# Kernel optimization log

Hardware: AMD Instinct MI355X
Metric: run time of the kernel (lower is better)

Reference implementation:

```python
import jax, jax.numpy as jnp
import numpy as np

N_USERS = 100000
N_ENT = 100000
DIM = 64
HID = 128
E = 1600000
B = 8192


def _renorm(emb, max_norm=1.0):
    # torch nn.Embedding(max_norm=1): rows are rescaled to norm <= max_norm on lookup
    n = jnp.linalg.norm(emb, axis=-1, keepdims=True)
    return emb * jnp.minimum(1.0, max_norm / jnp.maximum(n, 1e-12))


def _gcn_conv(x, W, b, src, dst, n):
    # PyG GCNConv: h = x W; add self-loops; sym-normalized scatter-add; + bias
    h = x @ W  # [n, out]
    deg = jax.ops.segment_sum(jnp.ones(src.shape, jnp.float32), dst, num_segments=n) + 1.0  # self-loop
    dinv = jax.lax.rsqrt(deg)
    norm = (dinv[src] * dinv[dst])[:, None]  # [E,1]
    out = jax.ops.segment_sum(h[src] * norm, dst, num_segments=n)
    out = out + h * (1.0 / deg)[:, None]  # self-loop term: deg^-1/2 * deg^-1/2 = 1/deg
    return out + b


def setup_inputs() -> dict:
    key = jax.random.key(0)
    ks = jax.random.split(key, 8)
    return {
        "u": jax.random.randint(ks[0], (B,), 0, N_USERS),
        "i": jax.random.randint(ks[1], (B,), 0, N_ENT),
        "edges": jax.random.randint(ks[2], (2, E), 0, N_ENT),
        "user_emb": jax.random.normal(ks[3], (N_USERS, DIM), jnp.float32) * 0.1,
        "entity_emb": jax.random.normal(ks[4], (N_ENT, DIM), jnp.float32) * 0.1,
        "W1": jax.random.normal(ks[5], (DIM, HID), jnp.float32) * (1.0 / np.sqrt(DIM)),
        "b1": jnp.zeros((HID,), jnp.float32),
        "W2": jax.random.normal(ks[6], (HID, DIM), jnp.float32) * (1.0 / np.sqrt(HID)),
        "b2": jnp.zeros((DIM,), jnp.float32),
    }


def reference(u, i, edges, user_emb, entity_emb, W1, b1, W2, b2):
    src, dst = edges[0], edges[1]
    n = entity_emb.shape[0]
    x = _renorm(entity_emb)  # entitys(all_entitys_indexes) with max_norm=1
    x = jax.nn.relu(_gcn_conv(x, W1, b1, src, dst, n))  # dropout = identity (eval)
    x = _gcn_conv(x, W2, b2, src, dst, n)
    items = x[i]  # [B, DIM]
    users = _renorm(user_emb)[u]  # [B, DIM]
    uv = jnp.sum(users * items, axis=1)
    return jax.nn.sigmoid(uv)
```

## Files before the change

kernel.cpp:

```cpp
#include <hip/hip_runtime.h>
#include <hip/hip_bf16.h>
#include <math.h>

constexpr int N_ENT = 100000;
constexpr int NEDGE = 1600000;
constexpr int BATCH = 8192;

constexpr int NBUCK   = 256;
constexpr int KNODE   = 391;
constexpr int TILE    = 4096;
constexpr int NTILE   = (NEDGE + TILE - 1) / TILE;
constexpr int BUCKCAP = 8192;

constexpr int NBLK_G = (N_ENT + 63) / 64;
constexpr int ZROWS  = NBLK_G * 64;


typedef __attribute__((ext_vector_type(8))) short bf16x8;
typedef __attribute__((ext_vector_type(4))) float f32x4;

__device__ inline unsigned short f2b(float x) {
    unsigned int u = __float_as_uint(x);
    unsigned int r = (u + 0x7fffu + ((u >> 16) & 1u)) >> 16;
    return (unsigned short)r;
}
__device__ inline float blo(unsigned int p) { return __uint_as_float(p << 16); }
__device__ inline float bhi(unsigned int p) { return __uint_as_float(p & 0xffff0000u); }


__global__ __launch_bounds__(256) void ginit_k(int* __restrict__ gcursor) {
    gcursor[threadIdx.x] = threadIdx.x * BUCKCAP;
}

__global__ __launch_bounds__(256) void bin_k(const int* __restrict__ edges,
                                             int* __restrict__ gcursor,
                                             unsigned int* __restrict__ temp) {
    __shared__ int cnt[NBUCK];
    __shared__ int gb[NBUCK];
    __shared__ int off[NBUCK];
    int tid  = threadIdx.x;
    int base = blockIdx.x * TILE;
    unsigned int val[16];
    unsigned int bpk[4] = {0u, 0u, 0u, 0u};
    cnt[tid] = 0;
    __syncthreads();
#pragma unroll
    for (int i = 0; i < 16; ++i) {
        int e = base + i * 256 + tid;
        unsigned int b = 0u;
        if (e < NEDGE) {
            int s  = edges[e];
            int d  = edges[NEDGE + e];
            int bb = d / KNODE;
            int dl = d - bb * KNODE;
            val[i] = ((unsigned int)s << 9) | (unsigned int)dl;
            b = (unsigned int)bb;
            atomicAdd(&cnt[bb], 1);
        } else {
            val[i] = 0xffffffffu;
        }
        bpk[i >> 2] |= b << ((i & 3) * 8);
    }
    __syncthreads();
    if (cnt[tid] > 0) gb[tid] = atomicAdd(&gcursor[tid], cnt[tid]);
    off[tid] = 0;
    __syncthreads();
#pragma unroll
    for (int i = 0; i < 16; ++i) {
        if (val[i] != 0xffffffffu) {
            int b = (int)((bpk[i >> 2] >> ((i & 3) * 8)) & 255u);
            int p = atomicAdd(&off[b], 1);
            temp[gb[b] + p] = val[i];
        }
    }
}

__global__ __launch_bounds__(256) void unbinC_k(const unsigned int* __restrict__ temp,
                                                const int* __restrict__ gcursor,
                                                const float* __restrict__ W1g,
                                                const float* __restrict__ W2g,
                                                uint4* __restrict__ w1p,
                                                uint4* __restrict__ w2p,
                                                int* __restrict__ row_start,
                                                int* __restrict__ srcs) {
    __shared__ unsigned int st[BUCKCAP];
    __shared__ int bs[NBUCK];
    __shared__ int cnt[KNODE];
    __shared__ int cur[KNODE];
    int b   = blockIdx.x;
    int tid = threadIdx.x;
    if (b >= NBUCK) {
        int t    = (b - NBUCK) * 256 + tid;
        int e    = t & 1023;
        int lane = e & 63, cs = e >> 6;
        int li   = lane & 15, quad = lane >> 4;
        unsigned short v[8];
        if (t < 1024) {
            int ct = cs >> 1, s = cs & 1;
            int kb = s * 32 + quad * 8;
            int n  = ct * 16 + li;
#pragma unroll
            for (int j = 0; j < 8; ++j) v[j] = f2b(W1g[(kb + j) * 128 + n]);
            uint4 p;
            p.x = (unsigned)v[0] | ((unsigned)v[1] << 16);
            p.y = (unsigned)v[2] | ((unsigned)v[3] << 16);
            p.z = (unsigned)v[4] | ((unsigned)v[5] << 16);
            p.w = (unsigned)v[6] | ((unsigned)v[7] << 16);
            w1p[e] = p;
        } else {
            int ct = cs >> 2, s = cs & 3;
            int kb = s * 32 + quad * 8;
            int n  = ct * 16 + li;
#pragma unroll
            for (int j = 0; j < 8; ++j) v[j] = f2b(W2g[(kb + j) * 64 + n]);
            uint4 p;
            p.x = (unsigned)v[0] | ((unsigned)v[1] << 16);
            p.y = (unsigned)v[2] | ((unsigned)v[3] << 16);
            p.z = (unsigned)v[4] | ((unsigned)v[5] << 16);
            p.w = (unsigned)v[6] | ((unsigned)v[7] << 16);
            w2p[e] = p;
        }
        return;
    }
    int myc = gcursor[tid] - tid * BUCKCAP;
    bs[tid] = myc;
    __syncthreads();
    for (int off = 1; off < NBUCK; off <<= 1) {
        int x = (tid >= off) ? bs[tid - off] : 0;
        __syncthreads();
        bs[tid] += x;
        __syncthreads();
    }
    int node0 = b * KNODE;
    int nn    = N_ENT - node0; if (nn > KNODE) nn = KNODE;
    int tbeg  = b * BUCKCAP;
    int m     = gcursor[b] - tbeg;
    int bucket_base = bs[b] - m;
    for (int i = tid; i < KNODE; i += 256) cnt[i] = 0;
    __syncthreads();
    for (int i = tid; i < m; i += 256) {
        unsigned int x = temp[tbeg + i];
        st[i] = x;
        atomicAdd(&cnt[x & 511u], 1);
    }
    if (b == 0 && tid == 255) row_start[N_ENT] = NEDGE;
    __syncthreads();
    if (tid < 64) {
        int lane = tid;
        int loc[7];
        int s = 0;
#pragma unroll
        for (int j = 0; j < 7; ++j) {
            int idx = lane * 7 + j;
            int d = (idx < nn) ? cnt[idx] : 0;
            loc[j] = s;
            s += d;
        }
        int v = s;
#pragma unroll
        for (int o = 1; o < 64; o <<= 1) {
            int x = __shfl_up(v, o, 64);
            if (lane >= o) v += x;
        }
        int pfx = v - s;
#pragma unroll
        for (int j = 0; j < 7; ++j) {
            int idx = lane * 7 + j;
            if (idx < nn) {
                int rs = bucket_base + pfx + loc[j];
                cur[idx] = rs;
                row_start[node0 + idx] = rs;
            }
        }
    }
    __syncthreads();
    for (int i = tid; i < m; i += 256) {
        unsigned int x = st[i];
        int dl  = (int)(x & 511u);
        int pos = atomicAdd(&cur[dl], 1);
        srcs[pos] = (int)(x >> 9);
    }
}

__global__ __launch_bounds__(256) void prep_k(const float* __restrict__ emb,
                                              const int* __restrict__ row_start,
                                              float* __restrict__ dinv,
                                              unsigned short* __restrict__ emb_b) {
    int gt   = blockIdx.x * 256 + threadIdx.x;
    int n    = gt >> 6;
    int lane = threadIdx.x & 63;
    if (n > N_ENT) return;
    if (n == N_ENT) { emb_b[(size_t)n * 64 + lane] = 0; return; }
    float v = emb[(size_t)n * 64 + lane];
    float s = v * v;
#pragma unroll
    for (int o = 32; o > 0; o >>= 1) s += __shfl_xor(s, o, 64);
    float nrm = sqrtf(s);
    float sc  = nrm > 1.0f ? 1.0f / nrm : 1.0f;
    int   deg = row_start[n + 1] - row_start[n];
    float dv  = 1.0f / sqrtf((float)(deg + 1));
    if (lane == 0) dinv[n] = dv;
    emb_b[(size_t)n * 64 + lane] = f2b(sc * dv * v);
}

__global__ __launch_bounds__(256) void reduce1_k(int dst0,
                                                 const int* __restrict__ row_start,
                                                 const int* __restrict__ srcs,
                                                 const unsigned short* __restrict__ emb_b,
                                                 const float* __restrict__ dinv,
                                                 unsigned short* __restrict__ zb) {
    int gt   = blockIdx.x * 256 + threadIdx.x;
    int dst  = dst0 + (gt >> 6);
    int lane = threadIdx.x & 63;
    int sub  = lane >> 4;
    int li   = lane & 15;
    int beg = row_start[dst];
    int end = row_start[dst + 1];
    float4 acc = make_float4(0.f, 0.f, 0.f, 0.f);
    for (int base = beg; base < end; base += 64) {
        int cnt = end - base; if (cnt > 64) cnt = 64;
        int s_v = (base + lane < end) ? srcs[base + lane] : N_ENT;
        for (int jj = 0; jj < cnt; jj += 16) {
            int s0 = __shfl(s_v, jj + sub,      64);
            int s1 = __shfl(s_v, jj + 4 + sub,  64);
            int s2 = __shfl(s_v, jj + 8 + sub,  64);
            int s3 = __shfl(s_v, jj + 12 + sub, 64);
            uint2 p0 = *(const uint2*)(emb_b + (size_t)s0 * 64 + li * 4);
            uint2 p1 = *(const uint2*)(emb_b + (size_t)s1 * 64 + li * 4);
            uint2 p2 = *(const uint2*)(emb_b + (size_t)s2 * 64 + li * 4);
            uint2 p3 = *(const uint2*)(emb_b + (size_t)s3 * 64 + li * 4);
            acc.x += blo(p0.x) + blo(p1.x) + blo(p2.x) + blo(p3.x);
            acc.y += bhi(p0.x) + bhi(p1.x) + bhi(p2.x) + bhi(p3.x);
            acc.z += blo(p0.y) + blo(p1.y) + blo(p2.y) + blo(p3.y);
            acc.w += bhi(p0.y) + bhi(p1.y) + bhi(p2.y) + bhi(p3.y);
        }
    }
    acc.x += __shfl_xor(acc.x, 16, 64); acc.y += __shfl_xor(acc.y, 16, 64);
    acc.z += __shfl_xor(acc.z, 16, 64); acc.w += __shfl_xor(acc.w, 16, 64);
    acc.x += __shfl_xor(acc.x, 32, 64); acc.y += __shfl_xor(acc.y, 32, 64);
    acc.z += __shfl_xor(acc.z, 32, 64); acc.w += __shfl_xor(acc.w, 32, 64);
    if (lane < 16) {
        uint2 po = *(const uint2*)(emb_b + (size_t)dst * 64 + li * 4);
        float dv = dinv[dst];
        unsigned int h0 = f2b(dv * (acc.x + blo(po.x)));
        unsigned int h1 = f2b(dv * (acc.y + bhi(po.x)));
        unsigned int h2 = f2b(dv * (acc.z + blo(po.y)));
        unsigned int h3 = f2b(dv * (acc.w + bhi(po.y)));
        uint2 p;
        p.x = h0 | (h1 << 16);
        p.y = h2 | (h3 << 16);
        *(uint2*)(zb + (size_t)dst * 64 + li * 4) = p;
    }
}

__global__ __launch_bounds__(256) void mlp_k(const unsigned short* __restrict__ zb,
                                             const uint4* __restrict__ w1p,
                                             const float* __restrict__ b1,
                                             const uint4* __restrict__ w2p,
                                             const float* __restrict__ dinv,
                                             unsigned short* __restrict__ h2b) {
    __shared__ unsigned short y1s[4][16 * 136];
    __shared__ unsigned short h2s[4][16 * 64];
    int tid  = threadIdx.x;
    int w    = tid >> 6, lane = tid & 63;
    int li   = lane & 15, quad = lane >> 4;
    int r0   = blockIdx.x * 64 + w * 16;
    uint4 a0u = *(const uint4*)(zb + (size_t)(r0 + li) * 64 + quad * 8);
    uint4 a1u = *(const uint4*)(zb + (size_t)(r0 + li) * 64 + 32 + quad * 8);
    bf16x8 a0 = *(bf16x8*)&a0u;
    bf16x8 a1 = *(bf16x8*)&a1u;
    unsigned short* ys = y1s[w];
#pragma unroll
    for (int ct = 0; ct < 8; ++ct) {
        uint4 b0u = w1p[(ct * 2 + 0) * 64 + lane];
        uint4 b1u = w1p[(ct * 2 + 1) * 64 + lane];
        f32x4 acc = {0.f, 0.f, 0.f, 0.f};
        acc = __builtin_amdgcn_mfma_f32_16x16x32_bf16(a0, *(bf16x8*)&b0u, acc, 0, 0, 0);
        acc = __builtin_amdgcn_mfma_f32_16x16x32_bf16(a1, *(bf16x8*)&b1u, acc, 0, 0, 0);
        float bias = b1[ct * 16 + li];
#pragma unroll
        for (int r = 0; r < 4; ++r)
            ys[(quad * 4 + r) * 136 + ct * 16 + li] = f2b(fmaxf(acc[r] + bias, 0.f));
    }
    __syncthreads();
    bf16x8 a2[4];
#pragma unroll
    for (int s = 0; s < 4; ++s) {
        uint4 au = *(const uint4*)(ys + li * 136 + s * 32 + quad * 8);
        a2[s] = *(bf16x8*)&au;
    }
    float dvr[4];
#pragma unroll
    for (int r = 0; r < 4; ++r) {
        int grow = r0 + quad * 4 + r;
        dvr[r] = (grow < N_ENT) ? dinv[grow] : 0.f;
    }
    unsigned short* hs = h2s[w];
#pragma unroll
    for (int ct = 0; ct < 4; ++ct) {
        f32x4 acc = {0.f, 0.f, 0.f, 0.f};
#pragma unroll
        for (int s = 0; s < 4; ++s) {
            uint4 bu = w2p[(ct * 4 + s) * 64 + lane];
            acc = __builtin_amdgcn_mfma_f32_16x16x32_bf16(a2[s], *(bf16x8*)&bu, acc, 0, 0, 0);
        }
#pragma unroll
        for (int r = 0; r < 4; ++r)
            hs[(quad * 4 + r) * 64 + ct * 16 + li] = f2b(acc[r] * dvr[r]);
    }
    __syncthreads();
#pragma unroll
    for (int q = 0; q < 2; ++q) {
        int t4   = lane * 2 + q;
        int rl   = t4 >> 3;
        int c0   = (t4 & 7) * 8;
        int grow = r0 + rl;
        if (grow < N_ENT) {
            *(uint4*)(h2b + (size_t)grow * 64 + c0) = *(const uint4*)(hs + rl * 64 + c0);
        } else if (grow == N_ENT) {
            uint4 zz; zz.x = 0u; zz.y = 0u; zz.z = 0u; zz.w = 0u;
            *(uint4*)(h2b + (size_t)grow * 64 + c0) = zz;
        }
    }
}

__global__ __launch_bounds__(256) void reduce2f_k(const int* __restrict__ u,
                                                  const int* __restrict__ iidx,
                                                  const float* __restrict__ uemb,
                                                  const int* __restrict__ row_start,
                                                  const int* __restrict__ srcs,
                                                  const unsigned short* __restrict__ h2b,
                                                  const float* __restrict__ dinv,
                                                  const float* __restrict__ b2,
                                                  float* __restrict__ out) {
    int gt   = blockIdx.x * 256 + threadIdx.x;
    int b    = gt >> 6;
    int lane = threadIdx.x & 63;
    int sub  = lane >> 4;
    int li   = lane & 15;
    int dst = iidx[b];
    int beg = row_start[dst];
    int end = row_start[dst + 1];
    float4 acc = make_float4(0.f, 0.f, 0.f, 0.f);
    for (int base = beg; base < end; base += 64) {
        int cnt = end - base; if (cnt > 64) cnt = 64;
        int s_v = (base + lane < end) ? srcs[base + lane] : N_ENT;
        for (int jj = 0; jj < cnt; jj += 16) {
            int s0 = __shfl(s_v, jj + sub,      64);
            int s1 = __shfl(s_v, jj + 4 + sub,  64);
            int s2 = __shfl(s_v, jj + 8 + sub,  64);
            int s3 = __shfl(s_v, jj + 12 + sub, 64);
            uint2 p0 = *(const uint2*)(h2b + (size_t)s0 * 64 + li * 4);
            uint2 p1 = *(const uint2*)(h2b + (size_t)s1 * 64 + li * 4);
            uint2 p2 = *(const uint2*)(h2b + (size_t)s2 * 64 + li * 4);
            uint2 p3 = *(const uint2*)(h2b + (size_t)s3 * 64 + li * 4);
            acc.x += blo(p0.x) + blo(p1.x) + blo(p2.x) + blo(p3.x);
            acc.y += bhi(p0.x) + bhi(p1.x) + bhi(p2.x) + bhi(p3.x);
            acc.z += blo(p0.y) + blo(p1.y) + blo(p2.y) + blo(p3.y);
            acc.w += bhi(p0.y) + bhi(p1.y) + bhi(p2.y) + bhi(p3.y);
        }
    }
    acc.x += __shfl_xor(acc.x, 16, 64); acc.y += __shfl_xor(acc.y, 16, 64);
    acc.z += __shfl_xor(acc.z, 16, 64); acc.w += __shfl_xor(acc.w, 16, 64);
    acc.x += __shfl_xor(acc.x, 32, 64); acc.y += __shfl_xor(acc.y, 32, 64);
    acc.z += __shfl_xor(acc.z, 32, 64); acc.w += __shfl_xor(acc.w, 32, 64);
    float s1 = 0.f, s2 = 0.f;
    if (lane < 16) {
        uint2 po = *(const uint2*)(h2b + (size_t)dst * 64 + li * 4);
        float dv = dinv[dst];
        float4 bb = *(const float4*)(b2 + li * 4);
        float4 z2v;
        z2v.x = dv * (acc.x + blo(po.x)) + bb.x;
        z2v.y = dv * (acc.y + bhi(po.x)) + bb.y;
        z2v.z = dv * (acc.z + blo(po.y)) + bb.z;
        z2v.w = dv * (acc.w + bhi(po.y)) + bb.w;
        float4 ue = *(const float4*)(uemb + (size_t)u[b] * 64 + li * 4);
        s1 = ue.x * ue.x + ue.y * ue.y + ue.z * ue.z + ue.w * ue.w;
        s2 = ue.x * z2v.x + ue.y * z2v.y + ue.z * z2v.z + ue.w * z2v.w;
    }
#pragma unroll
    for (int o = 8; o > 0; o >>= 1) {
        s1 += __shfl_xor(s1, o, 64);
        s2 += __shfl_xor(s2, o, 64);
    }
    if (lane == 0) {
        float nrm = sqrtf(s1);
        float sc  = nrm > 1.0f ? 1.0f / nrm : 1.0f;
        float uv  = s2 * sc;
        out[b] = 1.0f / (1.0f + expf(-uv));
    }
}

extern "C" void kernel_launch(void* const* d_in, const int* in_sizes, int n_in,
                              void* d_out, int out_size, void* d_ws, size_t ws_size,
                              hipStream_t stream) {
    const int*   u          = (const int*)d_in[0];
    const int*   iidx       = (const int*)d_in[1];
    const int*   edges      = (const int*)d_in[2];
    const float* user_emb   = (const float*)d_in[3];
    const float* entity_emb = (const float*)d_in[4];
    const float* W1         = (const float*)d_in[5];
    const float* b1         = (const float*)d_in[6];
    const float* W2         = (const float*)d_in[7];
    const float* b2         = (const float*)d_in[8];
    float*       out        = (float*)d_out;

    char* ws = (char*)d_ws;
    float*          dinv      = (float*)         (ws + 100000u * 4);
    int*            row_start = (int*)           (ws + 200000u * 4);
    int*            gcursor   = (int*)           (ws + 300004u * 4);
    uint4*          w1p       = (uint4*)         (ws + 300656u * 4);
    uint4*          w2p       = (uint4*)         (ws + 304752u * 4);
    int*            srcs      = (int*)           (ws + 308848u * 4);
    unsigned short* emb_b     = (unsigned short*)(ws + 1908848u * 4);
    unsigned short* zb        = (unsigned short*)(ws + 3508864u * 4);
    unsigned short* h2b       = (unsigned short*)(ws + 6711936u * 4);
    unsigned int*   temp      = (unsigned int*)  (ws + 8311968u * 4);

    ginit_k<<<1, 256, 0, stream>>>(gcursor);
    bin_k<<<NTILE, 256, 0, stream>>>(edges, gcursor, temp);
    unbinC_k<<<NBUCK + 8, 256, 0, stream>>>(temp, gcursor, W1, W2, w1p, w2p,
                                            row_start, srcs);
    prep_k<<<N_ENT * 64 / 256 + 1, 256, 0, stream>>>(entity_emb, row_start,
                                                     dinv, emb_b);

    reduce1_k<<<12500, 256, 0, stream>>>(0,     row_start, srcs, emb_b, dinv, zb);
    reduce1_k<<<12500, 256, 0, stream>>>(50000, row_start, srcs, emb_b, dinv, zb);
    mlp_k<<<NBLK_G, 256, 0, stream>>>(zb, w1p, b1, w2p, dinv, h2b);

    reduce2f_k<<<BATCH * 64 / 256, 256, 0, stream>>>(u, iidx, user_emb, row_start,
                                                     srcs, h2b, dinv, b2, out);
}
```

Baseline: 234.2 us.

## Fuse graph preprocessing kernels into one cooperative kernel with grid syncs

Merges cursor init, edge binning, CSR build with weight packing, and embedding renorm/bf16 conversion into a single cooperative kernel separated by grid.sync barriers. It also merges the two reduce1 launches into one and vectorizes the prep stage to float4 loads. The aim is to cut kernel launch overhead and inter-kernel gaps. In exchange, the grid is limited to NTILE blocks that must all be co-resident, and the CSR phase runs on only a subset of them while the rest wait at the barrier.

After: 377.7 us. +61.3%, slower.

```diff
diff --git a/kernel.cpp b/kernel.cpp
--- a/kernel.cpp
+++ b/kernel.cpp
@@ -1,6 +1,9 @@
 #include <hip/hip_runtime.h>
 #include <hip/hip_bf16.h>
+#include <hip/hip_cooperative_groups.h>
 #include <math.h>
+
+namespace cg = cooperative_groups;
 
 constexpr int N_ENT = 100000;
 constexpr int NEDGE = 1600000;
@@ -13,7 +16,6 @@
 constexpr int BUCKCAP = 8192;
 
 constexpr int NBLK_G = (N_ENT + 63) / 64;
-constexpr int ZROWS  = NBLK_G * 64;
 
 
 typedef __attribute__((ext_vector_type(8))) short bf16x8;
@@ -28,68 +30,129 @@
 __device__ inline float bhi(unsigned int p) { return __uint_as_float(p & 0xffff0000u); }
 
 
-__global__ __launch_bounds__(256) void ginit_k(int* __restrict__ gcursor) {
-    gcursor[threadIdx.x] = threadIdx.x * BUCKCAP;
-}
-
-__global__ __launch_bounds__(256) void bin_k(const int* __restrict__ edges,
+__global__ __launch_bounds__(256) void pre_k(const int* __restrict__ edges,
+                                             const float* __restrict__ W1g,
+                                             const float* __restrict__ W2g,
+                                             uint4* __restrict__ w1p,
+                                             uint4* __restrict__ w2p,
                                              int* __restrict__ gcursor,
-                                             unsigned int* __restrict__ temp) {
-    __shared__ int cnt[NBUCK];
-    __shared__ int gb[NBUCK];
-    __shared__ int off[NBUCK];
-    int tid  = threadIdx.x;
-    int base = blockIdx.x * TILE;
-    unsigned int val[16];
-    unsigned int bpk[4] = {0u, 0u, 0u, 0u};
-    cnt[tid] = 0;
-    __syncthreads();
-#pragma unroll
-    for (int i = 0; i < 16; ++i) {
-        int e = base + i * 256 + tid;
-        unsigned int b = 0u;
-        if (e < NEDGE) {
-            int s  = edges[e];
-            int d  = edges[NEDGE + e];
-            int bb = d / KNODE;
-            int dl = d - bb * KNODE;
-            val[i] = ((unsigned int)s << 9) | (unsigned int)dl;
-            b = (unsigned int)bb;
-            atomicAdd(&cnt[bb], 1);
-        } else {
-            val[i] = 0xffffffffu;
-        }
-        bpk[i >> 2] |= b << ((i & 3) * 8);
-    }
-    __syncthreads();
-    if (cnt[tid] > 0) gb[tid] = atomicAdd(&gcursor[tid], cnt[tid]);
-    off[tid] = 0;
-    __syncthreads();
-#pragma unroll
-    for (int i = 0; i < 16; ++i) {
-        if (val[i] != 0xffffffffu) {
-            int b = (int)((bpk[i >> 2] >> ((i & 3) * 8)) & 255u);
-            int p = atomicAdd(&off[b], 1);
-            temp[gb[b] + p] = val[i];
-        }
-    }
-}
-
-__global__ __launch_bounds__(256) void unbinC_k(const unsigned int* __restrict__ temp,
-                                                const int* __restrict__ gcursor,
-                                                const float* __restrict__ W1g,
-                                                const float* __restrict__ W2g,
-                                                uint4* __restrict__ w1p,
-                                                uint4* __restrict__ w2p,
-                                                int* __restrict__ row_start,
-                                                int* __restrict__ srcs) {
+                                             unsigned int* __restrict__ temp,
+                                             int* __restrict__ row_start,
+                                             int* __restrict__ srcs,
+                                             const float* __restrict__ emb,
+                                             float* __restrict__ dinv,
+                                             unsigned short* __restrict__ emb_b) {
+    cg::grid_group grid = cg::this_grid();
     __shared__ unsigned int st[BUCKCAP];
-    __shared__ int bs[NBUCK];
-    __shared__ int cnt[KNODE];
-    __shared__ int cur[KNODE];
+    __shared__ int cntS[KNODE];
+    __shared__ int curS[KNODE];
+    __shared__ int bsS[NBUCK];
     int b   = blockIdx.x;
     int tid = threadIdx.x;
-    if (b >= NBUCK) {
+
+    if (b == 0) {
+        gcursor[tid] = tid * BUCKCAP;
+        if (tid == 0) row_start[N_ENT] = NEDGE;
+    }
+    grid.sync();
+
+    {
+        int base = b * TILE;
+        unsigned int val[16];
+        unsigned int bpk[4] = {0u, 0u, 0u, 0u};
+        cntS[tid] = 0;
+        __syncthreads();
+#pragma unroll
+        for (int i = 0; i < 16; ++i) {
+            int e = base + i * 256 + tid;
+            unsigned int bk = 0u;
+            if (e < NEDGE) {
+                int s  = edges[e];
+                int d  = edges[NEDGE + e];
+                int bb = d / KNODE;
+                int dl = d - bb * KNODE;
+                val[i] = ((unsigned int)s << 9) | (unsigned int)dl;
+                bk = (unsigned int)bb;
+                atomicAdd(&cntS[bb], 1);
+            } else {
+                val[i] = 0xffffffffu;
+            }
+            bpk[i >> 2] |= bk << ((i & 3) * 8);
+        }
+        __syncthreads();
+        if (cntS[tid] > 0) curS[tid] = atomicAdd(&gcursor[tid], cntS[tid]);
+        bsS[tid] = 0;
+        __syncthreads();
+#pragma unroll
+        for (int i = 0; i < 16; ++i) {
+            if (val[i] != 0xffffffffu) {
+                int bk = (int)((bpk[i >> 2] >> ((i & 3) * 8)) & 255u);
+                int p  = atomicAdd(&bsS[bk], 1);
+                temp[curS[bk] + p] = val[i];
+            }
+        }
+    }
+    grid.sync();
+
+    if (b < NBUCK) {
+        int myc = gcursor[tid] - tid * BUCKCAP;
+        bsS[tid] = myc;
+        __syncthreads();
+        for (int off = 1; off < NBUCK; off <<= 1) {
+            int x = (tid >= off) ? bsS[tid - off] : 0;
+            __syncthreads();
+            bsS[tid] += x;
+            __syncthreads();
+        }
+        int node0 = b * KNODE;
+        int nn    = N_ENT - node0; if (nn > KNODE) nn = KNODE;
+        int tbeg  = b * BUCKCAP;
+        int m     = gcursor[b] - tbeg;
+        int bucket_base = bsS[b] - m;
+        for (int i = tid; i < KNODE; i += 256) cntS[i] = 0;
+        __syncthreads();
+        for (int i = tid; i < m; i += 256) {
+            unsigned int x = temp[tbeg + i];
+            st[i] = x;
+            atomicAdd(&cntS[x & 511u], 1);
+        }
+        __syncthreads();
+        if (tid < 64) {
+            int lane = tid;
+            int loc[7];
+            int s = 0;
+#pragma unroll
+            for (int j = 0; j < 7; ++j) {
+                int idx = lane * 7 + j;
+                int d = (idx < nn) ? cntS[idx] : 0;
+                loc[j] = s;
+                s += d;
+            }
+            int v = s;
+#pragma unroll
+            for (int o = 1; o < 64; o <<= 1) {
+                int x = __shfl_up(v, o, 64);
+                if (lane >= o) v += x;
+            }
+            int pfx = v - s;
+#pragma unroll
+            for (int j = 0; j < 7; ++j) {
+                int idx = lane * 7 + j;
+                if (idx < nn) {
+                    int rs = bucket_base + pfx + loc[j];
+                    curS[idx] = rs;
+                    row_start[node0 + idx] = rs;
+                }
+            }
+        }
+        __syncthreads();
+        for (int i = tid; i < m; i += 256) {
+            unsigned int x = st[i];
+            int dl  = (int)(x & 511u);
+            int pos = atomicAdd(&curS[dl], 1);
+            srcs[pos] = (int)(x >> 9);
+        }
+    } else if (b < NBUCK + 8) {
         int t    = (b - NBUCK) * 256 + tid;
         int e    = t & 1023;
         int lane = e & 63, cs = e >> 6;
@@ -120,97 +183,54 @@
             p.w = (unsigned)v[6] | ((unsigned)v[7] << 16);
             w2p[e] = p;
         }
-        return;
-    }
-    int myc = gcursor[tid] - tid * BUCKCAP;
-    bs[tid] = myc;
-    __syncthreads();
-    for (int off = 1; off < NBUCK; off <<= 1) {
-        int x = (tid >= off) ? bs[tid - off] : 0;
-        __syncthreads();
-        bs[tid] += x;
-        __syncthreads();
-    }
-    int node0 = b * KNODE;
-    int nn    = N_ENT - node0; if (nn > KNODE) nn = KNODE;
-    int tbeg  = b * BUCKCAP;
-    int m     = gcursor[b] - tbeg;
-    int bucket_base = bs[b] - m;
-    for (int i = tid; i < KNODE; i += 256) cnt[i] = 0;
-    __syncthreads();
-    for (int i = tid; i < m; i += 256) {
-        unsigned int x = temp[tbeg + i];
-        st[i] = x;
-        atomicAdd(&cnt[x & 511u], 1);
-    }
-    if (b == 0 && tid == 255) row_start[N_ENT] = NEDGE;
-    __syncthreads();
-    if (tid < 64) {
-        int lane = tid;
-        int loc[7];
-        int s = 0;
-#pragma unroll
-        for (int j = 0; j < 7; ++j) {
-            int idx = lane * 7 + j;
-            int d = (idx < nn) ? cnt[idx] : 0;
-            loc[j] = s;
-            s += d;
-        }
-        int v = s;
-#pragma unroll
-        for (int o = 1; o < 64; o <<= 1) {
-            int x = __shfl_up(v, o, 64);
-            if (lane >= o) v += x;
-        }
-        int pfx = v - s;
-#pragma unroll
-        for (int j = 0; j < 7; ++j) {
-            int idx = lane * 7 + j;
-            if (idx < nn) {
-                int rs = bucket_base + pfx + loc[j];
-                cur[idx] = rs;
-                row_start[node0 + idx] = rs;
-            }
-        }
-    }
-    __syncthreads();
-    for (int i = tid; i < m; i += 256) {
-        unsigned int x = st[i];
-        int dl  = (int)(x & 511u);
-        int pos = atomicAdd(&cur[dl], 1);
-        srcs[pos] = (int)(x >> 9);
-    }
-}
-
-__global__ __launch_bounds__(256) void prep_k(const float* __restrict__ emb,
-                                              const int* __restrict__ row_start,
-                                              float* __restrict__ dinv,
-                                              unsigned short* __restrict__ emb_b) {
-    int gt   = blockIdx.x * 256 + threadIdx.x;
-    int n    = gt >> 6;
-    int lane = threadIdx.x & 63;
-    if (n > N_ENT) return;
-    if (n == N_ENT) { emb_b[(size_t)n * 64 + lane] = 0; return; }
-    float v = emb[(size_t)n * 64 + lane];
-    float s = v * v;
-#pragma unroll
-    for (int o = 32; o > 0; o >>= 1) s += __shfl_xor(s, o, 64);
-    float nrm = sqrtf(s);
-    float sc  = nrm > 1.0f ? 1.0f / nrm : 1.0f;
-    int   deg = row_start[n + 1] - row_start[n];
-    float dv  = 1.0f / sqrtf((float)(deg + 1));
-    if (lane == 0) dinv[n] = dv;
-    emb_b[(size_t)n * 64 + lane] = f2b(sc * dv * v);
-}
-
-__global__ __launch_bounds__(256) void reduce1_k(int dst0,
-                                                 const int* __restrict__ row_start,
+    }
+    grid.sync();
+
+    {
+        int lane  = tid & 63;
+        int qid   = lane >> 4, li = lane & 15;
+        int gw    = (b * 256 + tid) >> 6;
+        int nw    = (NTILE * 256) >> 6;
+        for (int n4 = gw; n4 <= N_ENT / 4; n4 += nw) {
+            int n = n4 * 4 + qid;
+            if (n > N_ENT) continue;
+            unsigned short* dst = emb_b + (size_t)n * 64 + li * 4;
+            if (n == N_ENT) {
+                uint2 z; z.x = 0u; z.y = 0u;
+                *(uint2*)dst = z;
+                continue;
+            }
+            float4 v = *(const float4*)(emb + (size_t)n * 64 + li * 4);
+            float s = v.x * v.x + v.y * v.y + v.z * v.z + v.w * v.w;
+            s += __shfl_xor(s, 1, 64);
+            s += __shfl_xor(s, 2, 64);
+            s += __shfl_xor(s, 4, 64);
+            s += __shfl_xor(s, 8, 64);
+            float nrm = sqrtf(s);
+            float sc  = nrm > 1.0f ? 1.0f / nrm : 1.0f;
+            int   deg = row_start[n + 1] - row_start[n];
+            float dv  = 1.0f / sqrtf((float)(deg + 1));
+            if (li == 0) dinv[n] = dv;
+            float mch = sc * dv;
+            unsigned int h0 = f2b(mch * v.x);
+            unsigned int h1 = f2b(mch * v.y);
+            unsigned int h2 = f2b(mch * v.z);
+            unsigned int h3 = f2b(mch * v.w);
+            uint2 p;
+            p.x = h0 | (h1 << 16);
+            p.y = h2 | (h3 << 16);
+            *(uint2*)dst = p;
+        }
+    }
+}
+
+__global__ __launch_bounds__(256) void reduce1_k(const int* __restrict__ row_start,
                                                  const int* __restrict__ srcs,
                                                  const unsigned short* __restrict__ emb_b,
                                                  const float* __restrict__ dinv,
                                                  unsigned short* __restrict__ zb) {
     int gt   = blockIdx.x * 256 + threadIdx.x;
-    int dst  = dst0 + (gt >> 6);
+    int dst  = gt >> 6;
     int lane = threadIdx.x & 63;
     int sub  = lane >> 4;
     int li   = lane & 15;
@@ -417,15 +437,25 @@
     unsigned short* h2b       = (unsigned short*)(ws + 6711936u * 4);
     unsigned int*   temp      = (unsigned int*)  (ws + 8311968u * 4);
 
-    ginit_k<<<1, 256, 0, stream>>>(gcursor);
-    bin_k<<<NTILE, 256, 0, stream>>>(edges, gcursor, temp);
-    unbinC_k<<<NBUCK + 8, 256, 0, stream>>>(temp, gcursor, W1, W2, w1p, w2p,
-                                            row_start, srcs);
-    prep_k<<<N_ENT * 64 / 256 + 1, 256, 0, stream>>>(entity_emb, row_start,
-                                                     dinv, emb_b);
-
-    reduce1_k<<<12500, 256, 0, stream>>>(0,     row_start, srcs, emb_b, dinv, zb);
-    reduce1_k<<<12500, 256, 0, stream>>>(50000, row_start, srcs, emb_b, dinv, zb);
+    {
+        void* args[12];
+        args[0]  = (void*)&edges;
+        args[1]  = (void*)&W1;
+        args[2]  = (void*)&W2;
+        args[3]  = (void*)&w1p;
+        args[4]  = (void*)&w2p;
+        args[5]  = (void*)&gcursor;
+        args[6]  = (void*)&temp;
+        args[7]  = (void*)&row_start;
+        args[8]  = (void*)&srcs;
+        args[9]  = (void*)&entity_emb;
+        args[10] = (void*)&dinv;
+        args[11] = (void*)&emb_b;
+        hipLaunchCooperativeKernel((void*)pre_k, dim3(NTILE), dim3(256),
+                                   args, 0, stream);
+    }
+
+    reduce1_k<<<N_ENT * 64 / 256, 256, 0, stream>>>(row_start, srcs, emb_b, dinv, zb);
     mlp_k<<<NBLK_G, 256, 0, stream>>>(zb, w1p, b1, w2p, dinv, h2b);
 
     reduce2f_k<<<BATCH * 64 / 256, 256, 0, stream>>>(u, iidx, user_emb, row_start,
```
